# Kernel tuning notes

Measured on AMD Instinct MI355X. Metric: run time of the kernel, lower is better.

The kernel has to match this reference:

```python
import jax, jax.numpy as jnp
import numpy as np

L = 2999          # sequence length (odd -> clean consider_pad branch)
D = 512           # hidden dim
NB = 16           # number of gaussian basis functions
PENALTY = 0.1
SIGMAS = np.array([0.1, 0.5], dtype=np.float32)
INV_SQRT_2PI = 1.0 / np.sqrt(2.0 * np.pi)


def _gaussian(x, mu, sigma):
    z = (x - mu) / sigma
    return INV_SQRT_2PI / sigma * jnp.exp(-0.5 * z * z)


def _make_basis():
    # torch.meshgrid(linspace(0,1,NB//len(sigmas)), sigmas) with 'ij' indexing, flattened
    base_mu = np.linspace(0.0, 1.0, NB // len(SIGMAS)).astype(np.float32)
    mus = np.repeat(base_mu, len(SIGMAS))          # (NB,)
    sigs = np.tile(SIGMAS, NB // len(SIGMAS))      # (NB,)
    return jnp.asarray(mus), jnp.asarray(sigs)


def _make_G(basis_mu, basis_sigma):
    # get_positions with consider_pad=True, odd L: positions over padded interval
    shift = 1.0 / L
    pos = jnp.linspace(-0.5 + shift, 1.5 - shift, 2 * L - 1)          # (P,)
    F = _gaussian(pos[None, :], basis_mu[:, None], basis_sigma[:, None])  # (NB, P)
    I = jnp.eye(NB, dtype=jnp.float32)
    G_full = F.T @ jnp.linalg.inv(F @ F.T + PENALTY * I)              # (P, NB)
    half = (L - 1) // 2
    return G_full[half:-half]                                          # (L, NB)


def setup_inputs() -> dict:
    key = jax.random.key(0)
    k1, k2, k3, k4 = jax.random.split(key, 4)
    B = 32
    query = jax.random.normal(k1, (B, 1, D), dtype=jnp.float32)
    keys = jax.random.normal(k2, (B, L, D), dtype=jnp.float32)
    values = jax.random.normal(k3, (B, L, D), dtype=jnp.float32)
    mask = jnp.ones((B, L), dtype=bool)
    W_enc = jax.random.normal(k4, (D, D), dtype=jnp.float32) / np.sqrt(D)
    basis_mu, basis_sigma = _make_basis()
    G = _make_G(basis_mu, basis_sigma)
    return {"query": query, "keys": keys, "values": values, "mask": mask,
            "W_enc": W_enc, "G": G, "basis_mu": basis_mu, "basis_sigma": basis_sigma}


def reference(query, keys, values, mask, W_enc, G, basis_mu, basis_sigma):
    # --- encoder: discrete bilinear attention -> disc_p, mu, variance ---
    q = query[:, 0, :]                                   # (B, D)
    scores = jnp.einsum('bld,de,be->bl', keys, W_enc, q) / jnp.sqrt(jnp.float32(D))
    scores = jnp.where(mask, scores, -jnp.inf)
    disc_p = jax.nn.softmax(scores, axis=-1)             # (B, L)
    # discrete positions (consider_pad=False branch): midpoints of [0,1]
    pshift = 1.0 / (2.0 * L)
    pos = jnp.linspace(pshift, 1.0 - pshift, L)          # (L,)
    mu = disc_p @ pos                                    # (B,)
    e2 = disc_p @ (pos * pos)
    variance = jnp.clip(e2 - mu * mu, 1e-7, None)
    sigma_sq = jnp.clip(variance, 1e-12, None)           # softmax: sigma_sq = variance
    # --- continuous softmax: r_j = E_{N(mu,sigma_sq)}[psi_j] = N(mu; mu_j, sigma_sq+sig_j^2)
    tot_var = sigma_sq[:, None] + basis_sigma[None, :] ** 2      # (B, NB)
    r = INV_SQRT_2PI / jnp.sqrt(tot_var) * jnp.exp(
        -0.5 * (mu[:, None] - basis_mu[None, :]) ** 2 / tot_var)  # (B, NB)
    # --- value function: B = values^T G (all sequences full length -> shared G)
    Bmat = jnp.einsum('bld,ln->bdn', values, G)          # (B, D, NB)
    c = jnp.einsum('bdn,bn->bd', Bmat, r)[:, None, :]    # (B, 1, D)
    return c
```

## Files before the change

### kernel.cpp

```cpp
#include <hip/hip_runtime.h>
#include <math.h>

#define LL 2999
#define DD 512
#define NBASIS 16
#define BB 32

#define NCH 64
#define LCH 47

static constexpr float INV_SQRT_2PI = 0.3989422804014327f;
static constexpr float INV_SQRT_D   = 0.044194173824159216f;

__global__ __launch_bounds__(256) void k_gemv_t(const float* __restrict__ q,
                                                const float* __restrict__ W,
                                                float* __restrict__ t) {
    int wid  = blockIdx.x * 4 + (threadIdx.x >> 6);
    int lane = threadIdx.x & 63;
    int b = wid >> 9;
    int d = wid & 511;
    const float4* wrow = (const float4*)(W + (size_t)d * DD);
    const float4* qrow = (const float4*)(q + (size_t)b * DD);
    float sum = 0.f;
    #pragma unroll
    for (int e = lane; e < DD / 4; e += 64) {
        float4 wv = wrow[e], qv = qrow[e];
        sum += wv.x * qv.x + wv.y * qv.y + wv.z * qv.z + wv.w * qv.w;
    }
    #pragma unroll
    for (int off = 32; off > 0; off >>= 1) sum += __shfl_xor(sum, off);
    if (lane == 0) t[(size_t)b * DD + d] = sum;
}

__global__ __launch_bounds__(256) void k_scores(
    const float* __restrict__ keys, const float* __restrict__ t_buf,
    float* __restrict__ scores)
{
    const int wid  = blockIdx.x * 4 + (threadIdx.x >> 6);
    const int lane = threadIdx.x & 63;
    const int rA   = wid * 2;
    const int rB   = rA + 1;
    const int bA   = rA / LL;
    const int bB   = rB / LL;

    const float4* kA = (const float4*)(keys + (size_t)rA * DD);
    const float4* kB = (const float4*)(keys + (size_t)rB * DD);
    const float4* tA = (const float4*)(t_buf + (size_t)bA * DD);

    float4 ka0 = kA[lane], ka1 = kA[lane + 64];
    float4 kb0 = kB[lane], kb1 = kB[lane + 64];
    float4 ta0 = tA[lane], ta1 = tA[lane + 64];
    float4 tb0, tb1;
    if (bB == bA) { tb0 = ta0; tb1 = ta1; }
    else {
        const float4* tB = (const float4*)(t_buf + (size_t)bB * DD);
        tb0 = tB[lane]; tb1 = tB[lane + 64];
    }

    float sA = ka0.x * ta0.x + ka0.y * ta0.y + ka0.z * ta0.z + ka0.w * ta0.w
             + ka1.x * ta1.x + ka1.y * ta1.y + ka1.z * ta1.z + ka1.w * ta1.w;
    float sB = kb0.x * tb0.x + kb0.y * tb0.y + kb0.z * tb0.z + kb0.w * tb0.w
             + kb1.x * tb1.x + kb1.y * tb1.y + kb1.z * tb1.z + kb1.w * tb1.w;
    #pragma unroll
    for (int off = 32; off > 0; off >>= 1) {
        sA += __shfl_xor(sA, off);
        sB += __shfl_xor(sB, off);
    }
    if (lane == 0) {
        scores[rA] = sA * INV_SQRT_D;
        scores[rB] = sB * INV_SQRT_D;
    }
}

__global__ __launch_bounds__(256) void k_stats(const float* __restrict__ scores,
                                               const float* __restrict__ bmu,
                                               const float* __restrict__ bsig,
                                               float* __restrict__ r) {
    __shared__ float sh[256];
    int b = blockIdx.x, t = threadIdx.x;
    const float* srow = scores + (size_t)b * LL;

    float loc[12];
    float mx = -INFINITY;
    #pragma unroll
    for (int i = 0; i < 12; ++i) {
        int l = t + i * 256;
        if (l < LL) { loc[i] = srow[l]; mx = fmaxf(mx, loc[i]); }
    }
    sh[t] = mx; __syncthreads();
    for (int s = 128; s > 0; s >>= 1) { if (t < s) sh[t] = fmaxf(sh[t], sh[t + s]); __syncthreads(); }
    mx = sh[0]; __syncthreads();

    const float pshift = 1.0f / (2.0f * LL);
    const float step   = (1.0f - 2.0f * pshift) / (LL - 1);
    float s0 = 0.f, s1 = 0.f, s2 = 0.f;
    #pragma unroll
    for (int i = 0; i < 12; ++i) {
        int l = t + i * 256;
        if (l < LL) {
            float e = expf(loc[i] - mx);
            float p = pshift + l * step;
            s0 += e; s1 += e * p; s2 += e * p * p;
        }
    }
    sh[t] = s0; __syncthreads();
    for (int s = 128; s > 0; s >>= 1) { if (t < s) sh[t] += sh[t + s]; __syncthreads(); }
    s0 = sh[0]; __syncthreads();
    sh[t] = s1; __syncthreads();
    for (int s = 128; s > 0; s >>= 1) { if (t < s) sh[t] += sh[t + s]; __syncthreads(); }
    s1 = sh[0]; __syncthreads();
    sh[t] = s2; __syncthreads();
    for (int s = 128; s > 0; s >>= 1) { if (t < s) sh[t] += sh[t + s]; __syncthreads(); }
    s2 = sh[0]; __syncthreads();

    if (t < NBASIS) {
        float mu  = s1 / s0;
        float e2  = s2 / s0;
        float var = fmaxf(e2 - mu * mu, 1e-7f);
        float sg  = bsig[t];
        float tv  = var + sg * sg;
        float dm  = mu - bmu[t];
        r[b * NBASIS + t] = INV_SQRT_2PI / sqrtf(tv) * expf(-0.5f * dm * dm / tv);
    }
}

__global__ __launch_bounds__(128, 4) void k_partial(
    const float* __restrict__ values, const float* __restrict__ G,
    const float* __restrict__ r_buf, float* __restrict__ part)
{
    const int b  = blockIdx.x >> 6;
    const int ch = blockIdx.x & (NCH - 1);
    const int l0 = ch * LCH;
    const int l1 = (l0 + LCH < LL) ? l0 + LCH : LL;
    const int t  = threadIdx.x;

    const float4* rb = (const float4*)(r_buf + b * NBASIS);
    float4 r0 = rb[0], r1 = rb[1], r2 = rb[2], r3 = rb[3];

    const float4* vb = (const float4*)(values + (size_t)b * LL * DD) + t;
    float4 acc = make_float4(0.f, 0.f, 0.f, 0.f);

    int l = l0;
    for (; l + 2 <= l1; l += 2) {
        float4 v0 = vb[(size_t)l * (DD / 4)];
        float4 v1 = vb[(size_t)(l + 1) * (DD / 4)];
        const float4* g0 = (const float4*)(G + l * NBASIS);
        const float4* g1 = (const float4*)(G + (l + 1) * NBASIS);
        float4 ga = g0[0], gb = g0[1], gc = g0[2], gd = g0[3];
        float4 ha = g1[0], hb = g1[1], hc = g1[2], hd = g1[3];
        float wa = ga.x * r0.x + ga.y * r0.y + ga.z * r0.z + ga.w * r0.w
                 + gb.x * r1.x + gb.y * r1.y + gb.z * r1.z + gb.w * r1.w;
        float wb = gc.x * r2.x + gc.y * r2.y + gc.z * r2.z + gc.w * r2.w
                 + gd.x * r3.x + gd.y * r3.y + gd.z * r3.z + gd.w * r3.w;
        float w0 = wa + wb;
        float wc = ha.x * r0.x + ha.y * r0.y + ha.z * r0.z + ha.w * r0.w
                 + hb.x * r1.x + hb.y * r1.y + hb.z * r1.z + hb.w * r1.w;
        float wd = hc.x * r2.x + hc.y * r2.y + hc.z * r2.z + hc.w * r2.w
                 + hd.x * r3.x + hd.y * r3.y + hd.z * r3.z + hd.w * r3.w;
        float w1 = wc + wd;
        acc.x += w0 * v0.x; acc.y += w0 * v0.y; acc.z += w0 * v0.z; acc.w += w0 * v0.w;
        acc.x += w1 * v1.x; acc.y += w1 * v1.y; acc.z += w1 * v1.z; acc.w += w1 * v1.w;
    }
    if (l < l1) {
        float4 v0 = vb[(size_t)l * (DD / 4)];
        const float4* g0 = (const float4*)(G + l * NBASIS);
        float4 ga = g0[0], gb = g0[1], gc = g0[2], gd = g0[3];
        float wa = ga.x * r0.x + ga.y * r0.y + ga.z * r0.z + ga.w * r0.w
                 + gb.x * r1.x + gb.y * r1.y + gb.z * r1.z + gb.w * r1.w;
        float wb = gc.x * r2.x + gc.y * r2.y + gc.z * r2.z + gc.w * r2.w
                 + gd.x * r3.x + gd.y * r3.y + gd.z * r3.z + gd.w * r3.w;
        float w0 = wa + wb;
        acc.x += w0 * v0.x; acc.y += w0 * v0.y; acc.z += w0 * v0.z; acc.w += w0 * v0.w;
    }
    ((float4*)(part + (size_t)blockIdx.x * DD))[t] = acc;
}

__global__ __launch_bounds__(256) void k_reduce(const float* __restrict__ part,
                                                float* __restrict__ out) {
    int idx = blockIdx.x * 256 + threadIdx.x;
    int b = idx >> 9;
    int d = idx & 511;
    const float* p = part + (size_t)b * NCH * DD + d;
    float sum = 0.f;
    #pragma unroll 8
    for (int ch = 0; ch < NCH; ++ch) sum += p[(size_t)ch * DD];
    out[idx] = sum;
}

extern "C" void kernel_launch(void* const* d_in, const int* in_sizes, int n_in,
                              void* d_out, int out_size, void* d_ws, size_t ws_size,
                              hipStream_t stream) {
    const float* query  = (const float*)d_in[0];
    const float* keys   = (const float*)d_in[1];
    const float* values = (const float*)d_in[2];
    const float* W_enc  = (const float*)d_in[4];
    const float* G      = (const float*)d_in[5];
    const float* bmu    = (const float*)d_in[6];
    const float* bsig   = (const float*)d_in[7];
    float* out = (float*)d_out;
    float* ws  = (float*)d_ws;

    float* t_buf  = ws;
    float* scores = ws + 16384;
    float* r_buf  = ws + 112352;
    float* part   = ws + 112864;

    k_gemv_t<<<(BB * DD) / 4, 256, 0, stream>>>(query, W_enc, t_buf);
    k_scores<<<11996, 256, 0, stream>>>(keys, t_buf, scores);
    k_stats<<<BB, 256, 0, stream>>>(scores, bmu, bsig, r_buf);
    k_partial<<<BB * NCH, 128, 0, stream>>>(values, G, r_buf, part);
    k_reduce<<<(BB * DD) / 256, 256, 0, stream>>>(part, out);
}
```

Baseline: 88.27 us.

## Precompute per-position weights G·r in stats kernel; split partial over two row halves

The stats kernel now also computes w[b,l] = sum_n G[l,n]·r[b,n] for every position and writes it to a workspace buffer. This removes the 16-wide G dot product that every partial block repeated for each row, so the partial kernel reads a single scalar weight per row. The partial kernel also goes to 256 threads, with two halves interleaving rows and combining through shared memory, to raise memory-level parallelism on the values stream. The cost is extra serial work in the 32-block stats kernel and an additional workspace round trip.

```diff
diff --git a/kernel.cpp b/kernel.cpp
--- a/kernel.cpp
+++ b/kernel.cpp
@@ -72,11 +72,13 @@
     }
 }
 
-__global__ __launch_bounds__(256) void k_stats(const float* __restrict__ scores,
-                                               const float* __restrict__ bmu,
-                                               const float* __restrict__ bsig,
-                                               float* __restrict__ r) {
+__global__ __launch_bounds__(256) void k_statsw(const float* __restrict__ scores,
+                                                const float* __restrict__ G,
+                                                const float* __restrict__ bmu,
+                                                const float* __restrict__ bsig,
+                                                float* __restrict__ wbuf) {
     __shared__ float sh[256];
+    __shared__ float shr[NBASIS];
     int b = blockIdx.x, t = threadIdx.x;
     const float* srow = scores + (size_t)b * LL;
 
@@ -120,59 +122,55 @@
         float sg  = bsig[t];
         float tv  = var + sg * sg;
         float dm  = mu - bmu[t];
-        r[b * NBASIS + t] = INV_SQRT_2PI / sqrtf(tv) * expf(-0.5f * dm * dm / tv);
-    }
-}
-
-__global__ __launch_bounds__(128, 4) void k_partial(
-    const float* __restrict__ values, const float* __restrict__ G,
-    const float* __restrict__ r_buf, float* __restrict__ part)
+        shr[t] = INV_SQRT_2PI / sqrtf(tv) * expf(-0.5f * dm * dm / tv);
+    }
+    __syncthreads();
+
+    float r0 = shr[0],  r1 = shr[1],  r2 = shr[2],  r3 = shr[3];
+    float r4 = shr[4],  r5 = shr[5],  r6 = shr[6],  r7 = shr[7];
+    float r8 = shr[8],  r9 = shr[9],  rA = shr[10], rB = shr[11];
+    float rC = shr[12], rD = shr[13], rE = shr[14], rF = shr[15];
+    for (int l = t; l < LL; l += 256) {
+        const float4* g4 = (const float4*)(G + l * NBASIS);
+        float4 a = g4[0], c = g4[1], e = g4[2], f = g4[3];
+        float w = a.x * r0 + a.y * r1 + a.z * r2 + a.w * r3
+                + c.x * r4 + c.y * r5 + c.z * r6 + c.w * r7
+                + e.x * r8 + e.y * r9 + e.z * rA + e.w * rB
+                + f.x * rC + f.y * rD + f.z * rE + f.w * rF;
+        wbuf[(size_t)b * LL + l] = w;
+    }
+}
+
+__global__ __launch_bounds__(256) void k_partial(
+    const float* __restrict__ values, const float* __restrict__ wbuf,
+    float* __restrict__ part)
 {
+    __shared__ float4 shv[128];
     const int b  = blockIdx.x >> 6;
     const int ch = blockIdx.x & (NCH - 1);
     const int l0 = ch * LCH;
     const int l1 = (l0 + LCH < LL) ? l0 + LCH : LL;
-    const int t  = threadIdx.x;
-
-    const float4* rb = (const float4*)(r_buf + b * NBASIS);
-    float4 r0 = rb[0], r1 = rb[1], r2 = rb[2], r3 = rb[3];
-
-    const float4* vb = (const float4*)(values + (size_t)b * LL * DD) + t;
+    const int h  = threadIdx.x >> 7;
+    const int dt = threadIdx.x & 127;
+
+    const float4* vb = (const float4*)(values + (size_t)b * LL * DD) + dt;
+    const float*  wr = wbuf + (size_t)b * LL;
+
     float4 acc = make_float4(0.f, 0.f, 0.f, 0.f);
-
-    int l = l0;
-    for (; l + 2 <= l1; l += 2) {
-        float4 v0 = vb[(size_t)l * (DD / 4)];
-        float4 v1 = vb[(size_t)(l + 1) * (DD / 4)];
-        const float4* g0 = (const float4*)(G + l * NBASIS);
-        const float4* g1 = (const float4*)(G + (l + 1) * NBASIS);
-        float4 ga = g0[0], gb = g0[1], gc = g0[2], gd = g0[3];
-        float4 ha = g1[0], hb = g1[1], hc = g1[2], hd = g1[3];
-        float wa = ga.x * r0.x + ga.y * r0.y + ga.z * r0.z + ga.w * r0.w
-                 + gb.x * r1.x + gb.y * r1.y + gb.z * r1.z + gb.w * r1.w;
-        float wb = gc.x * r2.x + gc.y * r2.y + gc.z * r2.z + gc.w * r2.w
-                 + gd.x * r3.x + gd.y * r3.y + gd.z * r3.z + gd.w * r3.w;
-        float w0 = wa + wb;
-        float wc = ha.x * r0.x + ha.y * r0.y + ha.z * r0.z + ha.w * r0.w
-                 + hb.x * r1.x + hb.y * r1.y + hb.z * r1.z + hb.w * r1.w;
-        float wd = hc.x * r2.x + hc.y * r2.y + hc.z * r2.z + hc.w * r2.w
-                 + hd.x * r3.x + hd.y * r3.y + hd.z * r3.z + hd.w * r3.w;
-        float w1 = wc + wd;
-        acc.x += w0 * v0.x; acc.y += w0 * v0.y; acc.z += w0 * v0.z; acc.w += w0 * v0.w;
-        acc.x += w1 * v1.x; acc.y += w1 * v1.y; acc.z += w1 * v1.z; acc.w += w1 * v1.w;
-    }
-    if (l < l1) {
-        float4 v0 = vb[(size_t)l * (DD / 4)];
-        const float4* g0 = (const float4*)(G + l * NBASIS);
-        float4 ga = g0[0], gb = g0[1], gc = g0[2], gd = g0[3];
-        float wa = ga.x * r0.x + ga.y * r0.y + ga.z * r0.z + ga.w * r0.w
-                 + gb.x * r1.x + gb.y * r1.y + gb.z * r1.z + gb.w * r1.w;
-        float wb = gc.x * r2.x + gc.y * r2.y + gc.z * r2.z + gc.w * r2.w
-                 + gd.x * r3.x + gd.y * r3.y + gd.z * r3.z + gd.w * r3.w;
-        float w0 = wa + wb;
-        acc.x += w0 * v0.x; acc.y += w0 * v0.y; acc.z += w0 * v0.z; acc.w += w0 * v0.w;
-    }
-    ((float4*)(part + (size_t)blockIdx.x * DD))[t] = acc;
+    #pragma unroll 4
+    for (int l = l0 + h; l < l1; l += 2) {
+        float4 v = vb[(size_t)l * (DD / 4)];
+        float  w = wr[l];
+        acc.x += w * v.x; acc.y += w * v.y; acc.z += w * v.z; acc.w += w * v.w;
+    }
+
+    if (h == 1) shv[dt] = acc;
+    __syncthreads();
+    if (h == 0) {
+        float4 s = shv[dt];
+        acc.x += s.x; acc.y += s.y; acc.z += s.z; acc.w += s.w;
+        ((float4*)(part + (size_t)blockIdx.x * DD))[dt] = acc;
+    }
 }
 
 __global__ __launch_bounds__(256) void k_reduce(const float* __restrict__ part,
@@ -202,12 +200,12 @@
 
     float* t_buf  = ws;
     float* scores = ws + 16384;
-    float* r_buf  = ws + 112352;
-    float* part   = ws + 112864;
+    float* w_buf  = ws + 112352;
+    float* part   = ws + 208320;
 
     k_gemv_t<<<(BB * DD) / 4, 256, 0, stream>>>(query, W_enc, t_buf);
     k_scores<<<11996, 256, 0, stream>>>(keys, t_buf, scores);
-    k_stats<<<BB, 256, 0, stream>>>(scores, bmu, bsig, r_buf);
-    k_partial<<<BB * NCH, 128, 0, stream>>>(values, G, r_buf, part);
+    k_statsw<<<BB, 256, 0, stream>>>(scores, G, bmu, bsig, w_buf);
+    k_partial<<<BB * NCH, 256, 0, stream>>>(values, w_buf, part);
     k_reduce<<<(BB * DD) / 256, 256, 0, stream>>>(part, out);
 }
```

New measurement: 95.06 us. 1.08x slower.
